# Performance work log

Measured on AMD Instinct MI355X. Metric: run time of the kernel, lower is better.

The kernel has to match this reference:

```python
import jax, jax.numpy as jnp
import numpy as np

B, C, D, S = 1024, 128, 16, 4        # nodes, channels (mul), irrep feature dim (0e+1o+2e+3o), species
K3, K2, K1 = 23, 5, 2                # generalized-CG path counts for correlation 3/2/1
OUT_DIMS = (1, 3)                    # target irreps 0e (dim 1) and 1o (dim 3)


def setup_inputs() -> dict:
    key = jax.random.key(0)
    ks = jax.random.split(key, 12)
    f = lambda k, s: jax.random.normal(k, s, dtype=jnp.float32)
    U_SCALE = 0.05  # keep corr-3 products numerically moderate (stand-in CG basis)
    return {
        "node_feats": f(ks[0], (B, C, D)),
        "u3_0": f(ks[1], (1, D, D, D, K3)) * U_SCALE,
        "u3_1": f(ks[2], (3, D, D, D, K3)) * U_SCALE,
        "u2_0": f(ks[3], (1, D, D, K2)) * U_SCALE,
        "u2_1": f(ks[4], (3, D, D, K2)) * U_SCALE,
        "u1_0": f(ks[5], (1, D, K1)) * U_SCALE,
        "u1_1": f(ks[6], (3, D, K1)) * U_SCALE,
        "w3": f(ks[7], (2, S, K3, C)) / np.sqrt(K3),
        "w2": f(ks[8], (2, S, K2, C)) / np.sqrt(K2),
        "w1": f(ks[9], (2, S, K1, C)) / np.sqrt(K1),
        "w_lin": f(ks[10], (2, C, C)),
        "node_species": jax.random.randint(ks[11], (B,), 0, S, dtype=jnp.int32),
    }


def _sym_contract(x, sp, u3, u2, u1, w3, w2, w1):
    """MACE symmetric contraction for one output irrep.
    x: (B,C,D); u3: (do,D,D,D,K3); u2: (do,D,D,K2); u1: (do,D,K1);
    w*: (S,K*,C) per-species path weights. Returns (B,C,do)."""
    onehot = jax.nn.one_hot(sp, S, dtype=x.dtype)        # (B,S)
    # corr-3 main term: fold species weights into the basis once (small: S*C*do*D^3)
    uw3 = jnp.einsum('oijlk,ekc->ecoijl', u3, w3)        # (S,C,do,D,D,D)
    do = u3.shape[0]
    out = jnp.zeros((x.shape[0], x.shape[1], do, D, D), x.dtype)
    for e in range(S):  # fixed small species loop (irregular per-species access)
        out = out + onehot[:, e][:, None, None, None, None] * \
            jnp.einsum('coijl,bcl->bcoij', uw3[e], x)
    # corr-2: add weighted basis, contract one feature axis
    c2 = jnp.einsum('oijk,bkc->bcoij', u2, w2[sp]) + out
    out = jnp.einsum('bcoij,bcj->bcoi', c2, x)
    # corr-1
    c1 = jnp.einsum('oik,bkc->bcoi', u1, w1[sp]) + out
    return jnp.einsum('bcoi,bci->bco', c1, x)            # (B,C,do)


def reference(node_feats, u3_0, u3_1, u2_0, u2_1, u1_0, u1_1, w3, w2, w1, w_lin, node_species):
    y0 = _sym_contract(node_feats, node_species, u3_0, u2_0, u1_0, w3[0], w2[0], w1[0])
    y1 = _sym_contract(node_feats, node_species, u3_1, u2_1, u1_1, w3[1], w2[1], w1[1])
    # equivariant Linear(target_irreps): mix multiplicity channels per irrep, 1/sqrt(fan_in)
    scale = 1.0 / jnp.sqrt(jnp.asarray(C, node_feats.dtype))
    z0 = jnp.einsum('bco,cn->bno', y0, w_lin[0]) * scale  # (B,C,1)
    z1 = jnp.einsum('bco,cn->bno', y1, w_lin[1]) * scale  # (B,C,3)
    # axis_to_mul flattening: (B, C*1 + C*3)
    return jnp.concatenate([z0.reshape(B, C * 1), z1.reshape(B, C * 3)], axis=1)
```

## Files before the change

kernel.cpp:

```cpp
#include <hip/hip_runtime.h>
#include <hip/hip_bf16.h>

#define SS 4
#define CC 128
#define WELEM 18432
#define NK3 23
#define NK2 5
#define NK1 2

typedef unsigned int uint;
typedef unsigned short ushort;
typedef __attribute__((ext_vector_type(8))) short bf16x8;
typedef __attribute__((ext_vector_type(4))) float f32x4;

__device__ __forceinline__ ushort f2bf(float f) {
  uint u = __float_as_uint(f);
  return (ushort)((u + 0x7fffu + ((u >> 16) & 1u)) >> 16);
}
__device__ __forceinline__ uint pk2(float a, float b) {
  __hip_bfloat162 h = __float22bfloat162_rn(make_float2(a, b));
  return *(uint*)&h;
}

__global__ __launch_bounds__(256) void pre_kernel(
    const float* __restrict__ u3_0, const float* __restrict__ u3_1,
    const float* __restrict__ w3,
    const float* __restrict__ u2_0, const float* __restrict__ u2_1,
    const float* __restrict__ u1_0, const float* __restrict__ u1_1,
    const float* __restrict__ w2,  const float* __restrict__ w1,
    const int* __restrict__ sp, ushort* __restrict__ W,
    int* __restrict__ sorted, int* __restrict__ seg) {
  __shared__ float smem[5888 + NK3 * 64];
  int bx = blockIdx.x;
  int tid = threadIdx.x;

  if (bx < 512) {
    float* u3s = smem;
    float* w3s = smem + 5888;
    int ch = bx & 1, i = (bx >> 1) & 15, o = (bx >> 5) & 3, s = bx >> 7;
    int g = (o > 0) ? 1 : 0, og = g ? (o - 1) : 0;
    const float* u3 = g ? u3_1 : u3_0;

    const float4* u3p = (const float4*)(u3 + (size_t)(og * 16 + i) * 5888);
    for (int d = tid; d < 1472; d += 256) {
      float4 v = u3p[d];
      u3s[4 * d] = v.x; u3s[4 * d + 1] = v.y; u3s[4 * d + 2] = v.z; u3s[4 * d + 3] = v.w;
    }
    for (int t = tid; t < NK3 * 64; t += 256) {
      int k = t >> 6, cp = t & 63;
      w3s[t] = w3[((size_t)(g * SS + s) * NK3 + k) * CC + ch * 64 + cp];
    }
    __syncthreads();

    float acc[64];
    #pragma unroll
    for (int q = 0; q < 64; q++) acc[q] = 0.f;
    int jl = tid;
    for (int k = 0; k < NK3; k++) {
      float u3v = u3s[jl * NK3 + k];
      const float4* wp = (const float4*)&w3s[k * 64];
      #pragma unroll
      for (int cq = 0; cq < 16; cq++) {
        float4 wv = wp[cq];
        acc[cq * 4 + 0] = fmaf(u3v, wv.x, acc[cq * 4 + 0]);
        acc[cq * 4 + 1] = fmaf(u3v, wv.y, acc[cq * 4 + 1]);
        acc[cq * 4 + 2] = fmaf(u3v, wv.z, acc[cq * 4 + 2]);
        acc[cq * 4 + 3] = fmaf(u3v, wv.w, acc[cq * 4 + 3]);
      }
    }
    int n = o * 16 + i;
    #pragma unroll
    for (int cp = 0; cp < 64; cp++) {
      W[(size_t)(s * CC + ch * 64 + cp) * WELEM + n * 256 + jl] = f2bf(acc[cp]);
    }
  } else if (bx < 1024) {
    int b2 = bx - 512;
    int s = b2 >> 7, c = b2 & 127;
    int n = tid >> 2, lq = tid & 3;
    int o = n >> 4, i = n & 15;
    int g = (o > 0) ? 1 : 0, og = g ? (o - 1) : 0;
    const float* u2 = g ? u2_1 : u2_0;
    const float* u1 = g ? u1_1 : u1_0;

    float vals[8];
    #pragma unroll
    for (int t = 0; t < 8; t++) {
      int k = 256 + lq * 8 + t;
      float v = 0.f;
      if (k < 272) {
        int j = k - 256;
        #pragma unroll
        for (int k2 = 0; k2 < NK2; k2++)
          v = fmaf(u2[((size_t)(og * 16 + i) * 16 + j) * NK2 + k2],
                   w2[((size_t)(g * SS + s) * NK2 + k2) * CC + c], v);
      } else if (k == 272) {
        #pragma unroll
        for (int k2 = 0; k2 < NK1; k2++)
          v = fmaf(u1[(size_t)(og * 16 + i) * NK1 + k2],
                   w1[((size_t)(g * SS + s) * NK1 + k2) * CC + c], v);
      }
      vals[t] = v;
    }
    uint4 pk;
    pk.x = pk2(vals[0], vals[1]); pk.y = pk2(vals[2], vals[3]);
    pk.z = pk2(vals[4], vals[5]); pk.w = pk2(vals[6], vals[7]);
    size_t base = (size_t)(s * CC + c) * WELEM;
    size_t off = 16384 + ((size_t)o * 64 + lq * 16 + i) * 8;
    *(uint4*)(W + base + off) = pk;
  } else {
    __shared__ int cnt[SS];
    __shared__ int basep[SS + 1];
    if (tid < SS) cnt[tid] = 0;
    __syncthreads();
    int mysp[4], mypos[4];
    #pragma unroll
    for (int q = 0; q < 4; q++) {
      int node = q * 256 + tid;
      int s = sp[node];
      mysp[q] = s;
      mypos[q] = atomicAdd(&cnt[s], 1);
    }
    __syncthreads();
    if (tid == 0) {
      basep[0] = 0;
      for (int q = 0; q < SS; q++) basep[q + 1] = basep[q] + cnt[q];
      for (int q = 0; q <= SS; q++) seg[q] = basep[q];
    }
    __syncthreads();
    #pragma unroll
    for (int q = 0; q < 4; q++)
      sorted[basep[mysp[q]] + mypos[q]] = q * 256 + tid;
  }
}

__global__ __launch_bounds__(256, 2) void corr_kernel(
    const float* __restrict__ xg, const ushort* __restrict__ Wg,
    const int* __restrict__ sorted, const int* __restrict__ seg,
    float* __restrict__ y) {
  __shared__ uint4 Wl4[1536];
  __shared__ float xl[4][16][20];
  int bx = blockIdx.x;
  int s = bx >> 7, c = bx & 127;
  int tid = threadIdx.x;
  int w = tid >> 6, lane = tid & 63;
  int lq = lane >> 4, ln = lane & 15;

  const uint4* wg = (const uint4*)(Wg + (size_t)(s * CC + c) * WELEM);

  for (int d = tid; d < 1280; d += 256) {
    int n = d / 20, j = d % 20;
    int kt = 3 + (j >> 2), lqj = j & 3;
    int span = (kt - 3) * 4 + (n >> 4);
    int pos = (lqj * 16 + (n & 15)) ^ (kt & 7);
    Wl4[span * 64 + pos] = wg[n * 32 + 12 + j];
  }
  {
    int d = tid;
    Wl4[1280 + d] = wg[2048 + d];
  }
  uint4 Bc[12];
  #pragma unroll
  for (int kt = 0; kt < 3; kt++)
    #pragma unroll
    for (int nt = 0; nt < 4; nt++)
      Bc[kt * 4 + nt] = wg[(nt * 16 + ln) * 32 + kt * 4 + lq];

  int s0 = seg[s], s1 = seg[s + 1];
  __syncthreads();

  for (int base = s0; base < s1; base += 64) {
    int row = base + w * 16 + ln;
    int sval = (row < s1) ? sorted[row] : sorted[s0];
    float4 xc = *((const float4*)(xg + ((size_t)sval * CC + c) * 16) + lq);
    *(float4*)(&xl[w][ln][lq * 4]) = xc;
    float xv[16];
    #pragma unroll
    for (int q = 0; q < 4; q++) {
      float4 v = *(const float4*)(&xl[w][ln][q * 4]);
      xv[q * 4] = v.x; xv[q * 4 + 1] = v.y; xv[q * 4 + 2] = v.z; xv[q * 4 + 3] = v.w;
    }
    float xs8[8];
    #pragma unroll
    for (int t = 0; t < 8; t++) xs8[t] = (lq & 1) ? xv[8 + t] : xv[t];

    f32x4 acc[4];
    #pragma unroll
    for (int nt = 0; nt < 4; nt++) acc[nt] = (f32x4){0.f, 0.f, 0.f, 0.f};

    #pragma unroll
    for (int kt = 0; kt < 9; kt++) {
      uint4 av;
      if (kt < 8) {
        float xj = (lq & 2) ? xv[kt * 2 + 1] : xv[kt * 2];
        av.x = pk2(xj * xs8[0], xj * xs8[1]);
        av.y = pk2(xj * xs8[2], xj * xs8[3]);
        av.z = pk2(xj * xs8[4], xj * xs8[5]);
        av.w = pk2(xj * xs8[6], xj * xs8[7]);
      } else {
        av.x = pk2(xs8[0], xs8[1]);
        av.y = pk2(xs8[2], xs8[3]);
        av.z = pk2(xs8[4], xs8[5]);
        av.w = pk2(xs8[6], xs8[7]);
        if (lq == 2) av = make_uint4(0x3f80u, 0u, 0u, 0u);
        if (lq == 3) av = make_uint4(0u, 0u, 0u, 0u);
      }
      bf16x8 a = *(bf16x8*)&av;
      #pragma unroll
      for (int nt = 0; nt < 4; nt++) {
        uint4 bv;
        if (kt < 3) {
          bv = Bc[kt * 4 + nt];
        } else if (kt < 8) {
          bv = Wl4[((kt - 3) * 4 + nt) * 64 + (lane ^ (kt & 7))];
        } else {
          bv = Wl4[1280 + nt * 64 + lane];
        }
        bf16x8 b = *(bf16x8*)&bv;
        acc[nt] = __builtin_amdgcn_mfma_f32_16x16x32_bf16(a, b, acc[nt], 0, 0, 0);
      }
    }
    float xr[4];
    #pragma unroll
    for (int r = 0; r < 4; r++) xr[r] = xl[w][lq * 4 + r][ln];
    #pragma unroll
    for (int nt = 0; nt < 4; nt++) {
      #pragma unroll
      for (int r = 0; r < 4; r++) {
        float v = acc[nt][r] * xr[r];
        v += __shfl_xor(v, 1, 64);
        v += __shfl_xor(v, 2, 64);
        v += __shfl_xor(v, 4, 64);
        v += __shfl_xor(v, 8, 64);
        int m = lq * 4 + r;
        if (ln == m && (base + w * 16 + m) < s1) {
          y[((size_t)sval * CC + c) * 4 + nt] = v;
        }
      }
    }
  }
}

__global__ __launch_bounds__(128) void lin_kernel(
    const float* __restrict__ y, const float* __restrict__ w_lin,
    float* __restrict__ out) {
  int b = blockIdx.x;
  int n = threadIdx.x;
  const float4* yb4 = (const float4*)(y + (size_t)b * 512);
  float a0 = 0.f, a1 = 0.f, a2 = 0.f, a3 = 0.f;
  #pragma unroll 8
  for (int cc = 0; cc < CC; cc++) {
    float4 yv = yb4[cc];
    float wl0 = w_lin[(size_t)cc * CC + n];
    float wl1 = w_lin[16384 + (size_t)cc * CC + n];
    a0 = fmaf(yv.x, wl0, a0);
    a1 = fmaf(yv.y, wl1, a1);
    a2 = fmaf(yv.z, wl1, a2);
    a3 = fmaf(yv.w, wl1, a3);
  }
  const float scale = 0.08838834764831845f;
  out[(size_t)b * 512 + n] = a0 * scale;
  out[(size_t)b * 512 + 128 + (size_t)n * 3 + 0] = a1 * scale;
  out[(size_t)b * 512 + 128 + (size_t)n * 3 + 1] = a2 * scale;
  out[(size_t)b * 512 + 128 + (size_t)n * 3 + 2] = a3 * scale;
}

extern "C" void kernel_launch(void* const* d_in, const int* in_sizes, int n_in,
                              void* d_out, int out_size, void* d_ws, size_t ws_size,
                              hipStream_t stream) {
  const float* node_feats = (const float*)d_in[0];
  const float* u3_0 = (const float*)d_in[1];
  const float* u3_1 = (const float*)d_in[2];
  const float* u2_0 = (const float*)d_in[3];
  const float* u2_1 = (const float*)d_in[4];
  const float* u1_0 = (const float*)d_in[5];
  const float* u1_1 = (const float*)d_in[6];
  const float* w3   = (const float*)d_in[7];
  const float* w2   = (const float*)d_in[8];
  const float* w1   = (const float*)d_in[9];
  const float* wlin = (const float*)d_in[10];
  const int* species = (const int*)d_in[11];
  float* out = (float*)d_out;

  char* ws = (char*)d_ws;
  ushort* W  = (ushort*)ws;
  float* yb  = (float*)(ws + 18874368);
  int* sorted = (int*)(ws + 20971520);
  int* seg    = (int*)(ws + 20975616);

  pre_kernel<<<1025, 256, 0, stream>>>(u3_0, u3_1, w3, u2_0, u2_1, u1_0, u1_1,
                                       w2, w1, species, W, sorted, seg);
  corr_kernel<<<512, 256, 0, stream>>>(node_feats, W, sorted, seg, yb);
  lin_kernel<<<1024, 128, 0, stream>>>(yb, wlin, out);
}
```

Measured before the change: 129.4 us.

## Split corr kernel slabs across two block halves, prefetch x, LDS-based epilogue

The corr kernel grid doubles so that each (species, channel) pair gets two blocks, and those blocks take alternating 64-node slabs. Node features for the next slab are loaded into registers ahead of time, and the launch bound is raised to allow more blocks per CU. The shuffle-reduction epilogue is replaced: accumulators are written to LDS as bf16, then each lane does a 16-term dot product with x in registers. This cuts shuffle work but rounds the intermediate to bf16, and each block still reloads the W slab on its own.

```diff
diff --git a/kernel.cpp b/kernel.cpp
--- a/kernel.cpp
+++ b/kernel.cpp
@@ -7,12 +7,15 @@
 #define NK3 23
 #define NK2 5
 #define NK1 2
+#define DLP 72
 
 typedef unsigned int uint;
 typedef unsigned short ushort;
 typedef __attribute__((ext_vector_type(8))) short bf16x8;
 typedef __attribute__((ext_vector_type(4))) float f32x4;
 
+__device__ __forceinline__ float bflo(uint u){ return __uint_as_float(u << 16); }
+__device__ __forceinline__ float bfhi(uint u){ return __uint_as_float(u & 0xffff0000u); }
 __device__ __forceinline__ ushort f2bf(float f) {
   uint u = __float_as_uint(f);
   return (ushort)((u + 0x7fffu + ((u >> 16) & 1u)) >> 16);
@@ -133,14 +136,14 @@
   }
 }
 
-__global__ __launch_bounds__(256, 2) void corr_kernel(
+__global__ __launch_bounds__(256, 4) void corr_kernel(
     const float* __restrict__ xg, const ushort* __restrict__ Wg,
     const int* __restrict__ sorted, const int* __restrict__ seg,
     float* __restrict__ y) {
   __shared__ uint4 Wl4[1536];
-  __shared__ float xl[4][16][20];
+  __shared__ __align__(16) ushort Dl[4 * 16 * DLP];
   int bx = blockIdx.x;
-  int s = bx >> 7, c = bx & 127;
+  int h = bx >> 9, s = (bx >> 7) & 3, c = bx & 127;
   int tid = threadIdx.x;
   int w = tid >> 6, lane = tid & 63;
   int lq = lane >> 4, ln = lane & 15;
@@ -154,10 +157,7 @@
     int pos = (lqj * 16 + (n & 15)) ^ (kt & 7);
     Wl4[span * 64 + pos] = wg[n * 32 + 12 + j];
   }
-  {
-    int d = tid;
-    Wl4[1280 + d] = wg[2048 + d];
-  }
+  Wl4[1280 + tid] = wg[2048 + tid];
   uint4 Bc[12];
   #pragma unroll
   for (int kt = 0; kt < 3; kt++)
@@ -168,17 +168,34 @@
   int s0 = seg[s], s1 = seg[s + 1];
   __syncthreads();
 
-  for (int base = s0; base < s1; base += 64) {
-    int row = base + w * 16 + ln;
-    int sval = (row < s1) ? sorted[row] : sorted[s0];
-    float4 xc = *((const float4*)(xg + ((size_t)sval * CC + c) * 16) + lq);
-    *(float4*)(&xl[w][ln][lq * 4]) = xc;
+  int nslab = (s1 - s0 + 63) >> 6;
+  int kslab = h;
+  int sval = 0;
+  float4 xc[4];
+  if (kslab < nslab) {
+    int row = s0 + kslab * 64 + w * 16 + ln;
+    sval = sorted[min(row, s1 - 1)];
+    const float4* xp = (const float4*)(xg + ((size_t)sval * CC + c) * 16);
+    xc[0] = xp[0]; xc[1] = xp[1]; xc[2] = xp[2]; xc[3] = xp[3];
+  }
+
+  for (; kslab < nslab; kslab += 2) {
     float xv[16];
     #pragma unroll
     for (int q = 0; q < 4; q++) {
-      float4 v = *(const float4*)(&xl[w][ln][q * 4]);
-      xv[q * 4] = v.x; xv[q * 4 + 1] = v.y; xv[q * 4 + 2] = v.z; xv[q * 4 + 3] = v.w;
-    }
+      xv[q * 4] = xc[q].x; xv[q * 4 + 1] = xc[q].y;
+      xv[q * 4 + 2] = xc[q].z; xv[q * 4 + 3] = xc[q].w;
+    }
+    int svc = sval;
+    int rowc = s0 + kslab * 64 + w * 16 + ln;
+    int kn = kslab + 2;
+    if (kn < nslab) {
+      int row = s0 + kn * 64 + w * 16 + ln;
+      sval = sorted[min(row, s1 - 1)];
+      const float4* xp = (const float4*)(xg + ((size_t)sval * CC + c) * 16);
+      xc[0] = xp[0]; xc[1] = xp[1]; xc[2] = xp[2]; xc[3] = xp[3];
+    }
+
     float xs8[8];
     #pragma unroll
     for (int t = 0; t < 8; t++) xs8[t] = (lq & 1) ? xv[8 + t] : xv[t];
@@ -219,24 +236,25 @@
         acc[nt] = __builtin_amdgcn_mfma_f32_16x16x32_bf16(a, b, acc[nt], 0, 0, 0);
       }
     }
-    float xr[4];
-    #pragma unroll
-    for (int r = 0; r < 4; r++) xr[r] = xl[w][lq * 4 + r][ln];
-    #pragma unroll
-    for (int nt = 0; nt < 4; nt++) {
+
+    #pragma unroll
+    for (int nt = 0; nt < 4; nt++)
       #pragma unroll
-      for (int r = 0; r < 4; r++) {
-        float v = acc[nt][r] * xr[r];
-        v += __shfl_xor(v, 1, 64);
-        v += __shfl_xor(v, 2, 64);
-        v += __shfl_xor(v, 4, 64);
-        v += __shfl_xor(v, 8, 64);
-        int m = lq * 4 + r;
-        if (ln == m && (base + w * 16 + m) < s1) {
-          y[((size_t)sval * CC + c) * 4 + nt] = v;
-        }
-      }
-    }
+      for (int r = 0; r < 4; r++)
+        Dl[(w * 16 + lq * 4 + r) * DLP + nt * 16 + ln] = f2bf(acc[nt][r]);
+    const uint4* dp = (const uint4*)&Dl[(w * 16 + ln) * DLP + lq * 16];
+    uint4 d0 = dp[0], d1 = dp[1];
+    float r = 0.f;
+    r = fmaf(bflo(d0.x), xv[0],  r); r = fmaf(bfhi(d0.x), xv[1],  r);
+    r = fmaf(bflo(d0.y), xv[2],  r); r = fmaf(bfhi(d0.y), xv[3],  r);
+    r = fmaf(bflo(d0.z), xv[4],  r); r = fmaf(bfhi(d0.z), xv[5],  r);
+    r = fmaf(bflo(d0.w), xv[6],  r); r = fmaf(bfhi(d0.w), xv[7],  r);
+    r = fmaf(bflo(d1.x), xv[8],  r); r = fmaf(bfhi(d1.x), xv[9],  r);
+    r = fmaf(bflo(d1.y), xv[10], r); r = fmaf(bfhi(d1.y), xv[11], r);
+    r = fmaf(bflo(d1.z), xv[12], r); r = fmaf(bfhi(d1.z), xv[13], r);
+    r = fmaf(bflo(d1.w), xv[14], r); r = fmaf(bfhi(d1.w), xv[15], r);
+    if (rowc < s1)
+      y[((size_t)svc * CC + c) * 4 + lq] = r;
   }
 }
 
@@ -289,6 +307,6 @@
 
   pre_kernel<<<1025, 256, 0, stream>>>(u3_0, u3_1, w3, u2_0, u2_1, u1_0, u1_1,
                                        w2, w1, species, W, sorted, seg);
-  corr_kernel<<<512, 256, 0, stream>>>(node_feats, W, sorted, seg, yb);
+  corr_kernel<<<1024, 256, 0, stream>>>(node_feats, W, sorted, seg, yb);
   lin_kernel<<<1024, 128, 0, stream>>>(yb, wlin, out);
 }
```

After: 195.3 us. 50.9% more time.

## Swap MFMA operand roles so each wave keeps its weight slice in registers

Applied to the files above, without the earlier changes.

Reorganizes the correlation kernel so the folded weights become the MFMA A operand, held per wave in registers: one wave per output component, 16 rows each. The x-products become the B operand across 16 nodes. The precompute kernel's weight layout changes to a row-major 288-element stride to match. This removes the LDS staging, the __syncthreads and the 4-way per-node shuffle reductions. The grid doubles by splitting each species' node groups across two blocks for more parallelism, at the cost of reloading the weights per block and doing more x loads per lane.

```diff
diff --git a/kernel.cpp b/kernel.cpp
--- a/kernel.cpp
+++ b/kernel.cpp
@@ -3,6 +3,7 @@
 
 #define SS 4
 #define CC 128
+#define KROW 288
 #define WELEM 18432
 #define NK3 23
 #define NK2 5
@@ -71,7 +72,7 @@
     int n = o * 16 + i;
     #pragma unroll
     for (int cp = 0; cp < 64; cp++) {
-      W[(size_t)(s * CC + ch * 64 + cp) * WELEM + n * 256 + jl] = f2bf(acc[cp]);
+      W[(size_t)(s * CC + ch * 64 + cp) * WELEM + n * KROW + jl] = f2bf(acc[cp]);
     }
   } else if (bx < 1024) {
     int b2 = bx - 512;
@@ -104,9 +105,7 @@
     uint4 pk;
     pk.x = pk2(vals[0], vals[1]); pk.y = pk2(vals[2], vals[3]);
     pk.z = pk2(vals[4], vals[5]); pk.w = pk2(vals[6], vals[7]);
-    size_t base = (size_t)(s * CC + c) * WELEM;
-    size_t off = 16384 + ((size_t)o * 64 + lq * 16 + i) * 8;
-    *(uint4*)(W + base + off) = pk;
+    *(uint4*)(W + (size_t)(s * CC + c) * WELEM + n * KROW + 256 + lq * 8) = pk;
   } else {
     __shared__ int cnt[SS];
     __shared__ int basep[SS + 1];
@@ -137,106 +136,81 @@
     const float* __restrict__ xg, const ushort* __restrict__ Wg,
     const int* __restrict__ sorted, const int* __restrict__ seg,
     float* __restrict__ y) {
-  __shared__ uint4 Wl4[1536];
-  __shared__ float xl[4][16][20];
   int bx = blockIdx.x;
-  int s = bx >> 7, c = bx & 127;
+  int h = bx >> 9, s = (bx >> 7) & 3, c = bx & 127;
   int tid = threadIdx.x;
   int w = tid >> 6, lane = tid & 63;
   int lq = lane >> 4, ln = lane & 15;
 
-  const uint4* wg = (const uint4*)(Wg + (size_t)(s * CC + c) * WELEM);
-
-  for (int d = tid; d < 1280; d += 256) {
-    int n = d / 20, j = d % 20;
-    int kt = 3 + (j >> 2), lqj = j & 3;
-    int span = (kt - 3) * 4 + (n >> 4);
-    int pos = (lqj * 16 + (n & 15)) ^ (kt & 7);
-    Wl4[span * 64 + pos] = wg[n * 32 + 12 + j];
-  }
-  {
-    int d = tid;
-    Wl4[1280 + d] = wg[2048 + d];
-  }
-  uint4 Bc[12];
-  #pragma unroll
-  for (int kt = 0; kt < 3; kt++)
-    #pragma unroll
-    for (int nt = 0; nt < 4; nt++)
-      Bc[kt * 4 + nt] = wg[(nt * 16 + ln) * 32 + kt * 4 + lq];
+  const ushort* wa = Wg + (size_t)(s * CC + c) * WELEM + (w * 16 + ln) * KROW + lq * 8;
+  uint4 A0 = *(const uint4*)(wa);
+  uint4 A1 = *(const uint4*)(wa + 32);
+  uint4 A2 = *(const uint4*)(wa + 64);
+  uint4 A3 = *(const uint4*)(wa + 96);
+  uint4 A4 = *(const uint4*)(wa + 128);
+  uint4 A5 = *(const uint4*)(wa + 160);
+  uint4 A6 = *(const uint4*)(wa + 192);
+  uint4 A7 = *(const uint4*)(wa + 224);
+  uint4 A8 = *(const uint4*)(wa + 256);
 
   int s0 = seg[s], s1 = seg[s + 1];
-  __syncthreads();
-
-  for (int base = s0; base < s1; base += 64) {
-    int row = base + w * 16 + ln;
-    int sval = (row < s1) ? sorted[row] : sorted[s0];
-    float4 xc = *((const float4*)(xg + ((size_t)sval * CC + c) * 16) + lq);
-    *(float4*)(&xl[w][ln][lq * 4]) = xc;
+  int ngroup = (s1 - s0 + 15) >> 4;
+  int gh = (ngroup + 1) >> 1;
+  int g0 = h * gh, g1 = min(ngroup, g0 + gh);
+
+  for (int t = g0; t < g1; t++) {
+    int row = s0 + t * 16 + ln;
+    int sv = sorted[min(row, s1 - 1)];
+    const float4* xp = (const float4*)(xg + ((size_t)sv * CC + c) * 16);
+    float4 x0 = xp[0], x1 = xp[1], x2 = xp[2], x3 = xp[3];
     float xv[16];
-    #pragma unroll
-    for (int q = 0; q < 4; q++) {
-      float4 v = *(const float4*)(&xl[w][ln][q * 4]);
-      xv[q * 4] = v.x; xv[q * 4 + 1] = v.y; xv[q * 4 + 2] = v.z; xv[q * 4 + 3] = v.w;
-    }
+    xv[0] = x0.x; xv[1] = x0.y; xv[2]  = x0.z; xv[3]  = x0.w;
+    xv[4] = x1.x; xv[5] = x1.y; xv[6]  = x1.z; xv[7]  = x1.w;
+    xv[8] = x2.x; xv[9] = x2.y; xv[10] = x2.z; xv[11] = x2.w;
+    xv[12] = x3.x; xv[13] = x3.y; xv[14] = x3.z; xv[15] = x3.w;
+
     float xs8[8];
     #pragma unroll
-    for (int t = 0; t < 8; t++) xs8[t] = (lq & 1) ? xv[8 + t] : xv[t];
-
-    f32x4 acc[4];
-    #pragma unroll
-    for (int nt = 0; nt < 4; nt++) acc[nt] = (f32x4){0.f, 0.f, 0.f, 0.f};
+    for (int q = 0; q < 8; q++) xs8[q] = (lq & 1) ? xv[8 + q] : xv[q];
+
+    f32x4 acc = (f32x4){0.f, 0.f, 0.f, 0.f};
 
     #pragma unroll
     for (int kt = 0; kt < 9; kt++) {
-      uint4 av;
+      uint4 bv;
       if (kt < 8) {
         float xj = (lq & 2) ? xv[kt * 2 + 1] : xv[kt * 2];
-        av.x = pk2(xj * xs8[0], xj * xs8[1]);
-        av.y = pk2(xj * xs8[2], xj * xs8[3]);
-        av.z = pk2(xj * xs8[4], xj * xs8[5]);
-        av.w = pk2(xj * xs8[6], xj * xs8[7]);
+        bv.x = pk2(xj * xs8[0], xj * xs8[1]);
+        bv.y = pk2(xj * xs8[2], xj * xs8[3]);
+        bv.z = pk2(xj * xs8[4], xj * xs8[5]);
+        bv.w = pk2(xj * xs8[6], xj * xs8[7]);
       } else {
-        av.x = pk2(xs8[0], xs8[1]);
-        av.y = pk2(xs8[2], xs8[3]);
-        av.z = pk2(xs8[4], xs8[5]);
-        av.w = pk2(xs8[6], xs8[7]);
-        if (lq == 2) av = make_uint4(0x3f80u, 0u, 0u, 0u);
-        if (lq == 3) av = make_uint4(0u, 0u, 0u, 0u);
+        bv.x = pk2(xs8[0], xs8[1]);
+        bv.y = pk2(xs8[2], xs8[3]);
+        bv.z = pk2(xs8[4], xs8[5]);
+        bv.w = pk2(xs8[6], xs8[7]);
+        if (lq == 2) bv = make_uint4(0x3f80u, 0u, 0u, 0u);
+        if (lq == 3) bv = make_uint4(0u, 0u, 0u, 0u);
+      }
+      bf16x8 b = *(bf16x8*)&bv;
+      uint4 av;
+      switch (kt) {
+        case 0: av = A0; break; case 1: av = A1; break; case 2: av = A2; break;
+        case 3: av = A3; break; case 4: av = A4; break; case 5: av = A5; break;
+        case 6: av = A6; break; case 7: av = A7; break; default: av = A8; break;
       }
       bf16x8 a = *(bf16x8*)&av;
-      #pragma unroll
-      for (int nt = 0; nt < 4; nt++) {
-        uint4 bv;
-        if (kt < 3) {
-          bv = Bc[kt * 4 + nt];
-        } else if (kt < 8) {
-          bv = Wl4[((kt - 3) * 4 + nt) * 64 + (lane ^ (kt & 7))];
-        } else {
-          bv = Wl4[1280 + nt * 64 + lane];
-        }
-        bf16x8 b = *(bf16x8*)&bv;
-        acc[nt] = __builtin_amdgcn_mfma_f32_16x16x32_bf16(a, b, acc[nt], 0, 0, 0);
-      }
-    }
-    float xr[4];
-    #pragma unroll
-    for (int r = 0; r < 4; r++) xr[r] = xl[w][lq * 4 + r][ln];
-    #pragma unroll
-    for (int nt = 0; nt < 4; nt++) {
-      #pragma unroll
-      for (int r = 0; r < 4; r++) {
-        float v = acc[nt][r] * xr[r];
-        v += __shfl_xor(v, 1, 64);
-        v += __shfl_xor(v, 2, 64);
-        v += __shfl_xor(v, 4, 64);
-        v += __shfl_xor(v, 8, 64);
-        int m = lq * 4 + r;
-        if (ln == m && (base + w * 16 + m) < s1) {
-          y[((size_t)sval * CC + c) * 4 + nt] = v;
-        }
-      }
-    }
+      acc = __builtin_amdgcn_mfma_f32_16x16x32_bf16(a, b, acc, 0, 0, 0);
+    }
+
+    float p = acc[0] * xv[lq * 4 + 0];
+    p = fmaf(acc[1], xv[lq * 4 + 1], p);
+    p = fmaf(acc[2], xv[lq * 4 + 2], p);
+    p = fmaf(acc[3], xv[lq * 4 + 3], p);
+    p += __shfl_xor(p, 16, 64);
+    p += __shfl_xor(p, 32, 64);
+    if (lq == 0 && row < s1)
+      y[((size_t)sv * CC + c) * 4 + w] = p;
   }
 }
 
@@ -289,6 +263,6 @@
 
   pre_kernel<<<1025, 256, 0, stream>>>(u3_0, u3_1, w3, u2_0, u2_1, u1_0, u1_1,
                                        w2, w1, species, W, sorted, seg);
-  corr_kernel<<<512, 256, 0, stream>>>(node_feats, W, sorted, seg, yb);
+  corr_kernel<<<1024, 256, 0, stream>>>(node_feats, W, sorted, seg, yb);
   lin_kernel<<<1024, 128, 0, stream>>>(yb, wlin, out);
 }
```

Measured after the change: 158.2 us. +22.2%, slower.
